# Optimization experiments

Measured on AMD Instinct MI355X. Metric: run time of the kernel, lower is better.

## Reference

```python
import jax, jax.numpy as jnp
import numpy as np

B, S, M, E, H = 2, 2048, 2048, 1024, 16
D = E // H
LN_EPS = 1e-5


def setup_inputs() -> dict:
    key = jax.random.key(0)
    ks = jax.random.split(key, 14)
    w = lambda k: jax.random.normal(k, (E, E), dtype=jnp.float32) * 0.02
    return {
        "query": jax.random.normal(ks[0], (B, S, E), dtype=jnp.float32),
        "keys": jax.random.normal(ks[1], (B, M, E), dtype=jnp.float32),
        "values": jax.random.normal(ks[2], (B, M, E), dtype=jnp.float32),
        "Wq": w(ks[3]), "bq": jnp.zeros((E,), jnp.float32),
        "Wk": w(ks[4]), "bk": jnp.zeros((E,), jnp.float32),
        "Wv": w(ks[5]), "bv": jnp.zeros((E,), jnp.float32),
        "Wo": w(ks[6]), "bo": jnp.zeros((E,), jnp.float32),
        "gamma": jnp.ones((E,), jnp.float32),
        "beta": jnp.zeros((E,), jnp.float32),
    }


def reference(query, keys, values, Wq, bq, Wk, bk, Wv, bv, Wo, bo, gamma, beta):
    b, s, e = query.shape
    m = keys.shape[1]
    # projections (torch Linear: x @ W.T + b), split heads -> [b, H, len, D]
    Q = (jnp.einsum('bse,fe->bsf', query, Wq) + bq).reshape(b, s, H, D).transpose(0, 2, 1, 3)
    K = (jnp.einsum('bme,fe->bmf', keys, Wk) + bk).reshape(b, m, H, D).transpose(0, 2, 1, 3)
    V = (jnp.einsum('bme,fe->bmf', values, Wv) + bv).reshape(b, m, H, D).transpose(0, 2, 1, 3)
    scores = jnp.einsum('bhsd,bhmd->bhsm', Q, K) / np.sqrt(D).astype(np.float32)
    attn = jax.nn.softmax(scores, axis=-1)  # [b,H,s,m]; dropout is eval no-op
    attended = jnp.einsum('bhsm,bhmd->bhsd', attn, V)
    attended = attended.transpose(0, 2, 1, 3).reshape(b, s, e)
    y = jnp.einsum('bse,fe->bsf', attended, Wo) + bo + query
    mu = jnp.mean(y, axis=-1, keepdims=True)
    var = jnp.mean(jnp.square(y - mu), axis=-1, keepdims=True)
    out = (y - mu) * jax.lax.rsqrt(var + LN_EPS) * gamma + beta
    avg_attention = attn.mean(axis=1)  # [b,s,m]
    return out, avg_attention
```

## Files before the change

kernel.cpp:

```cpp
#include <hip/hip_runtime.h>
#include <hip/hip_bf16.h>

typedef unsigned short u16;
typedef unsigned int   u32;
typedef __attribute__((ext_vector_type(2)))  float fx2;
typedef __attribute__((ext_vector_type(4)))  float fx4;
typedef __attribute__((ext_vector_type(16))) float f32x16;
typedef __attribute__((ext_vector_type(4)))  u16   usx4;
typedef __attribute__((ext_vector_type(8)))  u16   usx8;
typedef __attribute__((ext_vector_type(8)))  __bf16 bf16x8;
typedef __attribute__((ext_vector_type(2)))  int   i32x2;
typedef __attribute__((ext_vector_type(2)))  u32   u32x2;

#define DEVI static __device__ __forceinline__

constexpr int Bb = 2, Ss = 2048, Mm = 2048, Ee = 1024, Hh = 16, Dd = 64;
#define QSCALE 0.18033688011112042f

DEVI u16 f2bf(float f) {
  u32 u = __builtin_bit_cast(u32, f);
  u32 r = (u + 0x7fffu + ((u >> 16) & 1u)) >> 16;
  return (u16)r;
}
DEVI bf16x8 as_bf(usx8 v) { return __builtin_bit_cast(bf16x8, v); }

DEVI void gld16(const u16* g, u16* l) {
  __builtin_amdgcn_global_load_lds((const __attribute__((address_space(1))) void*)g,
                                   (__attribute__((address_space(3))) void*)l, 16, 0, 0);
}

#if __has_builtin(__builtin_amdgcn_exp2f)
DEVI float xexp2(float x) { return __builtin_amdgcn_exp2f(x); }
#else
DEVI float xexp2(float x) { return exp2f(x); }
#endif

DEVI u32 cvtpk(float lo, float hi) {
  u32 r;
  asm("v_cvt_pk_bf16_f32 %0, %1, %2" : "=v"(r) : "v"(lo), "v"(hi));
  return r;
}
DEVI bf16x8 pa_from(u32 w0, u32 w1, u32 w2, u32 w3) {
  union { u32 u[4]; usx8 v; } t;
  t.u[0] = w0; t.u[1] = w1; t.u[2] = w2; t.u[3] = w3;
  return as_bf(t.v);
}

__global__ __launch_bounds__(256)
void gemm_qkv(const float* __restrict__ query, const float* __restrict__ keys,
              const float* __restrict__ values,
              const float* __restrict__ Wq, const float* __restrict__ bq,
              const float* __restrict__ Wk, const float* __restrict__ bk,
              const float* __restrict__ Wv, const float* __restrict__ bv,
              u16* __restrict__ Qbf, u16* __restrict__ Kbf, u16* __restrict__ Vt)
{
  __shared__ u16 As[2][128][40];
  __shared__ u16 Bs[2][64][40];
  const int tid = threadIdx.x;
  const int w = tid >> 6, l = tid & 63, g = l >> 4, ln = l & 15;
  const int wr = w >> 1, wc = w & 1;
  const int row0 = blockIdx.y * 128, col0 = blockIdx.x * 64;
  const int z = blockIdx.z;

  const float* A = (z == 0) ? query : (z == 1) ? keys : values;
  const float* W = (z == 0) ? Wq : (z == 1) ? Wk : Wv;
  const float* bias = (z == 0) ? bq : (z == 1) ? bk : bv;

  fx4 ra[4]; fx4 rb[2];
  auto g2r = [&](int kt) {
#pragma unroll
    for (int i = 0; i < 4; i++) {
      int f = tid + i * 256;
      int rr = f >> 3, c4 = f & 7;
      ra[i] = *(const fx4*)(A + (size_t)(row0 + rr) * 1024 + kt * 32 + c4 * 4);
    }
#pragma unroll
    for (int i = 0; i < 2; i++) {
      int f = tid + i * 256;
      int rr = f >> 3, c4 = f & 7;
      rb[i] = *(const fx4*)(W + (size_t)(col0 + rr) * 1024 + kt * 32 + c4 * 4);
    }
  };
  auto r2l = [&](int buf) {
#pragma unroll
    for (int i = 0; i < 4; i++) {
      int f = tid + i * 256;
      int rr = f >> 3, c4 = f & 7;
      u32x2 ua;
      ua[0] = cvtpk(ra[i][0], ra[i][1]); ua[1] = cvtpk(ra[i][2], ra[i][3]);
      *(u32x2*)&As[buf][rr][c4 * 4] = ua;
    }
#pragma unroll
    for (int i = 0; i < 2; i++) {
      int f = tid + i * 256;
      int rr = f >> 3, c4 = f & 7;
      u32x2 ub;
      ub[0] = cvtpk(rb[i][0], rb[i][1]); ub[1] = cvtpk(rb[i][2], rb[i][3]);
      *(u32x2*)&Bs[buf][rr][c4 * 4] = ub;
    }
  };

  fx4 acc[4][2];
#pragma unroll
  for (int i = 0; i < 4; i++)
#pragma unroll
    for (int j = 0; j < 2; j++) acc[i][j] = fx4{0.f, 0.f, 0.f, 0.f};

  g2r(0); r2l(0);
  const int NK = 1024 / 32;
  for (int kt = 0; kt < NK; kt++) {
    __syncthreads();
    if (kt + 1 < NK) g2r(kt + 1);
    const int buf = kt & 1;
    bf16x8 af[4], bfr[2];
#pragma unroll
    for (int mi = 0; mi < 4; mi++)
      af[mi] = as_bf(*(const usx8*)&As[buf][wr * 64 + mi * 16 + ln][g * 8]);
#pragma unroll
    for (int nj = 0; nj < 2; nj++)
      bfr[nj] = as_bf(*(const usx8*)&Bs[buf][wc * 32 + nj * 16 + ln][g * 8]);
    __builtin_amdgcn_s_setprio(1);
#pragma unroll
    for (int mi = 0; mi < 4; mi++)
#pragma unroll
      for (int nj = 0; nj < 2; nj++)
        acc[mi][nj] = __builtin_amdgcn_mfma_f32_16x16x32_bf16(af[mi], bfr[nj], acc[mi][nj], 0, 0, 0);
    __builtin_amdgcn_s_setprio(0);
    if (kt + 1 < NK) r2l((kt + 1) & 1);
  }

#pragma unroll
  for (int mi = 0; mi < 4; mi++) {
#pragma unroll
    for (int nj = 0; nj < 2; nj++) {
      const int j = col0 + wc * 32 + nj * 16 + ln;
      const float bj = bias[j];
      if (z == 2) {
        const int i0 = row0 + wr * 64 + mi * 16 + g * 4;
        const int b2 = i0 >> 11, m2 = i0 & 2047;
        const int h2 = j >> 6,  d2 = j & 63;
        u32x2 pk;
        pk[0] = cvtpk(acc[mi][nj][0] + bj, acc[mi][nj][1] + bj);
        pk[1] = cvtpk(acc[mi][nj][2] + bj, acc[mi][nj][3] + bj);
        *(u32x2*)&Vt[(((size_t)b2 * Hh + h2) * 64 + d2) * (size_t)Mm + m2] = pk;
      } else {
        u16* outp = (z == 0) ? Qbf : Kbf;
        const float sc = (z == 0) ? QSCALE : 1.0f;
#pragma unroll
        for (int r = 0; r < 4; r++) {
          const int i = row0 + wr * 64 + mi * 16 + g * 4 + r;
          outp[(size_t)i * 1024 + j] = f2bf((acc[mi][nj][r] + bj) * sc);
        }
      }
    }
  }
}

__global__ __launch_bounds__(256)
void gemm_out(const u16* __restrict__ Ab, const float* __restrict__ W,
              const float* __restrict__ bias, const float* __restrict__ resid,
              float* __restrict__ outf)
{
  __shared__ u16 As[2][128][40];
  __shared__ u16 Bs[2][64][40];
  const int tid = threadIdx.x;
  const int w = tid >> 6, l = tid & 63, g = l >> 4, ln = l & 15;
  const int wr = w >> 1, wc = w & 1;
  const int row0 = blockIdx.y * 128, col0 = blockIdx.x * 64;

  usx4 rau[4]; fx4 rb[2];
  auto g2r = [&](int kt) {
#pragma unroll
    for (int i = 0; i < 4; i++) {
      int f = tid + i * 256;
      int rr = f >> 3, c4 = f & 7;
      rau[i] = *(const usx4*)(Ab + (size_t)(row0 + rr) * 1024 + kt * 32 + c4 * 4);
    }
#pragma unroll
    for (int i = 0; i < 2; i++) {
      int f = tid + i * 256;
      int rr = f >> 3, c4 = f & 7;
      rb[i] = *(const fx4*)(W + (size_t)(col0 + rr) * 1024 + kt * 32 + c4 * 4);
    }
  };
  auto r2l = [&](int buf) {
#pragma unroll
    for (int i = 0; i < 4; i++) {
      int f = tid + i * 256;
      int rr = f >> 3, c4 = f & 7;
      *(usx4*)&As[buf][rr][c4 * 4] = rau[i];
    }
#pragma unroll
    for (int i = 0; i < 2; i++) {
      int f = tid + i * 256;
      int rr = f >> 3, c4 = f & 7;
      u32x2 ub;
      ub[0] = cvtpk(rb[i][0], rb[i][1]); ub[1] = cvtpk(rb[i][2], rb[i][3]);
      *(u32x2*)&Bs[buf][rr][c4 * 4] = ub;
    }
  };

  fx4 acc[4][2];
#pragma unroll
  for (int i = 0; i < 4; i++)
#pragma unroll
    for (int j = 0; j < 2; j++) acc[i][j] = fx4{0.f, 0.f, 0.f, 0.f};

  g2r(0); r2l(0);
  const int NK = 1024 / 32;
  for (int kt = 0; kt < NK; kt++) {
    __syncthreads();
    if (kt + 1 < NK) g2r(kt + 1);
    const int buf = kt & 1;
    bf16x8 af[4], bfr[2];
#pragma unroll
    for (int mi = 0; mi < 4; mi++)
      af[mi] = as_bf(*(const usx8*)&As[buf][wr * 64 + mi * 16 + ln][g * 8]);
#pragma unroll
    for (int nj = 0; nj < 2; nj++)
      bfr[nj] = as_bf(*(const usx8*)&Bs[buf][wc * 32 + nj * 16 + ln][g * 8]);
    __builtin_amdgcn_s_setprio(1);
#pragma unroll
    for (int mi = 0; mi < 4; mi++)
#pragma unroll
      for (int nj = 0; nj < 2; nj++)
        acc[mi][nj] = __builtin_amdgcn_mfma_f32_16x16x32_bf16(af[mi], bfr[nj], acc[mi][nj], 0, 0, 0);
    __builtin_amdgcn_s_setprio(0);
    if (kt + 1 < NK) r2l((kt + 1) & 1);
  }

#pragma unroll
  for (int mi = 0; mi < 4; mi++) {
#pragma unroll
    for (int nj = 0; nj < 2; nj++) {
      const int j = col0 + wc * 32 + nj * 16 + ln;
      const float bj = bias[j];
#pragma unroll
      for (int r = 0; r < 4; r++) {
        const int i = row0 + wr * 64 + mi * 16 + g * 4 + r;
        float v = acc[mi][nj][r] + bj + resid[(size_t)i * 1024 + j];
        outf[(size_t)i * 1024 + j] = v;
      }
    }
  }
}

__global__ __launch_bounds__(256, 2)
void flash_fwd(const u16* __restrict__ Qb, const u16* __restrict__ Kb,
               const u16* __restrict__ Vt, u16* __restrict__ attended,
               float* __restrict__ stats)
{
  __shared__ u16 Ks[2][128][64];
  __shared__ u16 Vs[2][64][128];
  const int tid = threadIdx.x;
  const int w = tid >> 6, l = tid & 63;
  const int ln32 = l & 31, hi = l >> 5;
  const int st = blockIdx.x, h = blockIdx.y, b = blockIdx.z;
  const int s0 = st * 128 + w * 32;

  const u16* Kbase = Kb + (size_t)b * Mm * 1024 + h * 64;
  const u16* Vbase = Vt + ((size_t)(b * Hh + h) * 64) * (size_t)Mm;

  const int colu_k = (((l & 7) ^ (l >> 3)) << 3);
  auto stage = [&](int buf, int mt) {
    const int mb = mt * 128;
#pragma unroll
    for (int j = 0; j < 4; j++) {
      const int c = j * 4 + w;
      const int krow = c * 8 + (l >> 3);
      gld16(Kbase + (size_t)(mb + krow) * 1024 + colu_k,
            &Ks[buf][0][0] + c * 512 + l * 8);
      const int vrow = c * 4 + (l >> 4);
      const int colv = (((l & 15) ^ (vrow & 15)) << 3);
      gld16(Vbase + (size_t)vrow * (size_t)Mm + mb + colv,
            &Vs[buf][0][0] + c * 512 + l * 8);
    }
  };

  bf16x8 qa[4];
#pragma unroll
  for (int dstep = 0; dstep < 4; dstep++)
    qa[dstep] = as_bf(*(const usx8*)(Qb + (size_t)(b * Ss + s0 + ln32) * Ee
                                     + h * 64 + dstep * 16 + hi * 8));

  f32x16 acc[2];
#pragma unroll
  for (int i = 0; i < 16; i++) { acc[0][i] = 0.f; acc[1][i] = 0.f; }
  float lsum = 0.f;

  stage(0, 0);
  __syncthreads();

  const int NT = Mm / 128;
  for (int mt = 0; mt < NT; mt++) {
    const int buf = mt & 1;
    if (mt + 1 < NT) stage(buf ^ 1, mt + 1);

    f32x16 sc[4];
#pragma unroll
    for (int mtile = 0; mtile < 4; mtile++) {
      const int row = mtile * 32 + ln32;
      const int sw = (row & 7) << 3;
      f32x16 c;
#pragma unroll
      for (int i = 0; i < 16; i++) c[i] = 0.f;
#pragma unroll
      for (int dstep = 0; dstep < 4; dstep++) {
        bf16x8 kf = as_bf(*(const usx8*)&Ks[buf][row][(dstep * 16 + hi * 8) ^ sw]);
        c = __builtin_amdgcn_mfma_f32_32x32x16_bf16(kf, qa[dstep], c, 0, 0, 0);
      }
      sc[mtile] = c;
    }

#pragma unroll
    for (int mtile = 0; mtile < 4; mtile++) {
      float p[16];
#pragma unroll
      for (int r = 0; r < 16; r++) p[r] = xexp2(sc[mtile][r]);
      float t0 = (p[0] + p[1]) + (p[2] + p[3]);
      float t1 = (p[4] + p[5]) + (p[6] + p[7]);
      float t2 = (p[8] + p[9]) + (p[10] + p[11]);
      float t3 = (p[12] + p[13]) + (p[14] + p[15]);
      lsum += (t0 + t1) + (t2 + t3);

      u32 cp[8];
#pragma unroll
      for (int i = 0; i < 8; i++) cp[i] = cvtpk(p[2 * i], p[2 * i + 1]);
      i32x2 sA = __builtin_amdgcn_permlane32_swap((int)cp[0], (int)cp[2], false, false);
      i32x2 sB = __builtin_amdgcn_permlane32_swap((int)cp[1], (int)cp[3], false, false);
      bf16x8 pa0 = pa_from((u32)sA.x, (u32)sB.x, (u32)sA.y, (u32)sB.y);
      i32x2 sC = __builtin_amdgcn_permlane32_swap((int)cp[4], (int)cp[6], false, false);
      i32x2 sD = __builtin_amdgcn_permlane32_swap((int)cp[5], (int)cp[7], false, false);
      bf16x8 pa1 = pa_from((u32)sC.x, (u32)sD.x, (u32)sC.y, (u32)sD.y);

#pragma unroll
      for (int dtile = 0; dtile < 2; dtile++) {
        const int vrow = dtile * 32 + ln32;
        const int vsw = (vrow & 15) << 3;
        bf16x8 vb0 = as_bf(*(const usx8*)&Vs[buf][vrow][(mtile * 32 + hi * 8) ^ vsw]);
        bf16x8 vb1 = as_bf(*(const usx8*)&Vs[buf][vrow][(mtile * 32 + 16 + hi * 8) ^ vsw]);
        acc[dtile] = __builtin_amdgcn_mfma_f32_32x32x16_bf16(pa0, vb0, acc[dtile], 0, 0, 0);
        acc[dtile] = __builtin_amdgcn_mfma_f32_32x32x16_bf16(pa1, vb1, acc[dtile], 0, 0, 0);
      }
    }
    __syncthreads();
  }

  lsum += __shfl_xor(lsum, 32);
  const float inv = 1.0f / lsum;
  if (l < 32)
    stats[(size_t)(b * Hh + h) * Ss + s0 + l] = inv;
#pragma unroll
  for (int r = 0; r < 16; r++) {
    const int srow = (r & 3) + 8 * (r >> 2) + 4 * hi;
    const float invr = __shfl(inv, srow);
    const int s_abs = s0 + srow;
#pragma unroll
    for (int dtile = 0; dtile < 2; dtile++)
      attended[(size_t)(b * Ss + s_abs) * Ee + h * 64 + dtile * 32 + ln32] =
          f2bf(acc[dtile][r] * invr);
  }
}

__global__ __launch_bounds__(256)
void avg_attn(const u16* __restrict__ Qb, const u16* __restrict__ Kb,
              const float* __restrict__ stats, float* __restrict__ avg_out)
{
  __shared__ u16 Ks[2][64][64];
  const int tid = threadIdx.x;
  const int w = tid >> 6, l = tid & 63;
  const int ln32 = l & 31, hi = l >> 5;
  const int mtile0 = blockIdx.x, stile = blockIdx.y, b = blockIdx.z;
  const int m0 = mtile0 * 64;
  const int s0 = stile * 128 + w * 32;
  const int s_lane = s0 + ln32;

  const u16* Kbase = Kb + (size_t)(b * Mm + m0) * 1024;
  const u16* Qrow  = Qb + (size_t)(b * Ss + s_lane) * Ee;
  const float* strow = stats + (size_t)b * Hh * Ss + s_lane;

  const int colu = (((l & 7) ^ (l >> 3)) << 3);
  auto stage = [&](int buf, int h) {
#pragma unroll
    for (int j = 0; j < 2; j++) {
      const int c = j * 4 + w;
      const int row = c * 8 + (l >> 3);
      u16* kdst = &Ks[buf][0][0] + c * 512 + l * 8;
      gld16(Kbase + (size_t)row * 1024 + h * 64 + colu, kdst);
    }
  };

  f32x16 acc[2];
#pragma unroll
  for (int i = 0; i < 16; i++) { acc[0][i] = 0.f; acc[1][i] = 0.f; }

  stage(0, 0);
  __syncthreads();

  for (int h = 0; h < Hh; h++) {
    const int buf = h & 1;
    if (h + 1 < Hh) stage(buf ^ 1, h + 1);

    bf16x8 qa[4];
#pragma unroll
    for (int dstep = 0; dstep < 4; dstep++)
      qa[dstep] = as_bf(*(const usx8*)(Qrow + h * 64 + dstep * 16 + hi * 8));
    const float invh = strow[(size_t)h * Ss];

#pragma unroll
    for (int mtile = 0; mtile < 2; mtile++) {
      const int row = mtile * 32 + ln32;
      const int sw = (row & 7) << 3;
      f32x16 c;
#pragma unroll
      for (int i = 0; i < 16; i++) c[i] = 0.f;
      __builtin_amdgcn_s_setprio(1);
#pragma unroll
      for (int dstep = 0; dstep < 4; dstep++) {
        bf16x8 kf = as_bf(*(const usx8*)&Ks[buf][row][(dstep * 16 + hi * 8) ^ sw]);
        c = __builtin_amdgcn_mfma_f32_32x32x16_bf16(kf, qa[dstep], c, 0, 0, 0);
      }
      __builtin_amdgcn_s_setprio(0);
#pragma unroll
      for (int r = 0; r < 16; r++)
        acc[mtile][r] += xexp2(c[r]) * invh;
    }
    __syncthreads();
  }

  float* orow = avg_out + ((size_t)(b * Ss + s_lane)) * Mm + m0;
#pragma unroll
  for (int mtile = 0; mtile < 2; mtile++)
#pragma unroll
    for (int rq = 0; rq < 4; rq++) {
      fx4 o;
#pragma unroll
      for (int j = 0; j < 4; j++) o[j] = acc[mtile][rq * 4 + j] * (1.0f / 16.0f);
      *(fx4*)(orow + mtile * 32 + rq * 8 + 4 * hi) = o;
    }
}

__global__ __launch_bounds__(256)
void ln_kernel(const float* __restrict__ y, const float* __restrict__ gamma,
               const float* __restrict__ beta, float* __restrict__ out)
{
  const int row = blockIdx.x, tid = threadIdx.x;
  const int w = tid >> 6, l = tid & 63;
  fx4 v = *(const fx4*)(y + (size_t)row * 1024 + tid * 4);
  float s = v[0] + v[1] + v[2] + v[3];
  float s2 = v[0] * v[0] + v[1] * v[1] + v[2] * v[2] + v[3] * v[3];
#pragma unroll
  for (int off = 32; off >= 1; off >>= 1) {
    s += __shfl_xor(s, off);
    s2 += __shfl_xor(s2, off);
  }
  __shared__ float rs[4], rq[4];
  if (l == 0) { rs[w] = s; rq[w] = s2; }
  __syncthreads();
  s = (rs[0] + rs[1]) + (rs[2] + rs[3]);
  s2 = (rq[0] + rq[1]) + (rq[2] + rq[3]);
  const float mu = s * (1.0f / 1024.0f);
  const float var = s2 * (1.0f / 1024.0f) - mu * mu;
  const float rstd = rsqrtf(var + 1e-5f);
  fx4 gm = *(const fx4*)(gamma + tid * 4);
  fx4 bt = *(const fx4*)(beta + tid * 4);
  fx4 o;
#pragma unroll
  for (int j = 0; j < 4; j++) o[j] = (v[j] - mu) * rstd * gm[j] + bt[j];
  *(fx4*)(out + (size_t)row * 1024 + tid * 4) = o;
}

extern "C" void kernel_launch(void* const* d_in, const int* in_sizes, int n_in,
                              void* d_out, int out_size, void* d_ws, size_t ws_size,
                              hipStream_t stream)
{
  const float* query = (const float*)d_in[0];
  const float* keys  = (const float*)d_in[1];
  const float* values = (const float*)d_in[2];
  const float* Wq = (const float*)d_in[3];  const float* bq = (const float*)d_in[4];
  const float* Wk = (const float*)d_in[5];  const float* bk = (const float*)d_in[6];
  const float* Wv = (const float*)d_in[7];  const float* bv = (const float*)d_in[8];
  const float* Wo = (const float*)d_in[9];  const float* bo = (const float*)d_in[10];
  const float* gamma = (const float*)d_in[11];
  const float* beta  = (const float*)d_in[12];

  float* out = (float*)d_out;
  float* avg_out = out + (size_t)Bb * Ss * Ee;

  char* ws = (char*)d_ws;
  u16*   Qbf      = (u16*)(ws);
  u16*   Kbf      = (u16*)(ws + (size_t)8  * 1024 * 1024);
  u16*   Vt       = (u16*)(ws + (size_t)16 * 1024 * 1024);
  u16*   att_bf   = (u16*)(ws + (size_t)24 * 1024 * 1024);
  float* stats    = (float*)(ws + (size_t)40 * 1024 * 1024);
  float* ybuf     = (float*)(ws);

  gemm_qkv<<<dim3(16, 32, 3), 256, 0, stream>>>(query, keys, values,
                                                Wq, bq, Wk, bk, Wv, bv,
                                                Qbf, Kbf, Vt);

  flash_fwd<<<dim3(Ss / 128, Hh, Bb), 256, 0, stream>>>(Qbf, Kbf, Vt, att_bf, stats);
  avg_attn<<<dim3(Mm / 64, Ss / 128, Bb), 256, 0, stream>>>(Qbf, Kbf, stats, avg_out);

  gemm_out<<<dim3(16, 32, 1), 256, 0, stream>>>(att_bf, Wo, bo, query, ybuf);
  ln_kernel<<<dim3(Bb * Ss), 256, 0, stream>>>(ybuf, gamma, beta, out);
}
```

Measured before the change: 189.6 us.

## Pre-cast inputs and weights to bf16, use direct-to-LDS loads with larger GEMM tiles

Adds a cast kernel that converts the activations and all four weight matrices to bf16 before the projections. The QKV and output GEMMs then stage tiles with global_load_lds into XOR-swizzled shared memory, move from 128x64 to 128x128 tiles with a K-step of 64, and remap block IDs to group the work. This removes the register round-trip and the per-tile fp32-to-bf16 conversion in the GEMM inner loops. In exchange it adds a separate pass that reads the fp32 inputs and writes bf16 copies, plus more workspace memory. The weights are re-cast on every call.

```diff
diff --git a/kernel.cpp b/kernel.cpp
--- a/kernel.cpp
+++ b/kernel.cpp
@@ -11,6 +11,7 @@
 typedef __attribute__((ext_vector_type(8)))  __bf16 bf16x8;
 typedef __attribute__((ext_vector_type(2)))  int   i32x2;
 typedef __attribute__((ext_vector_type(2)))  u32   u32x2;
+typedef __attribute__((ext_vector_type(4)))  u32   u32x4;
 
 #define DEVI static __device__ __forceinline__
 
@@ -47,93 +48,117 @@
 }
 
 __global__ __launch_bounds__(256)
-void gemm_qkv(const float* __restrict__ query, const float* __restrict__ keys,
-              const float* __restrict__ values,
-              const float* __restrict__ Wq, const float* __restrict__ bq,
-              const float* __restrict__ Wk, const float* __restrict__ bk,
-              const float* __restrict__ Wv, const float* __restrict__ bv,
+void cast_all(const float* __restrict__ q, const float* __restrict__ k,
+              const float* __restrict__ v,
+              const float* __restrict__ wq, const float* __restrict__ wk,
+              const float* __restrict__ wv, const float* __restrict__ wo,
+              u16* __restrict__ qc, u16* __restrict__ kc, u16* __restrict__ vc,
+              u16* __restrict__ wqc, u16* __restrict__ wkc,
+              u16* __restrict__ wvc, u16* __restrict__ woc)
+{
+  const int y = blockIdx.y;
+  const float* s; u16* d; size_t n;
+  const size_t NI = (size_t)Bb * Ss * Ee;
+  const size_t NW = (size_t)Ee * Ee;
+  switch (y) {
+    case 0: s = q;  d = qc;  n = NI; break;
+    case 1: s = k;  d = kc;  n = NI; break;
+    case 2: s = v;  d = vc;  n = NI; break;
+    case 3: s = wq; d = wqc; n = NW; break;
+    case 4: s = wk; d = wkc; n = NW; break;
+    case 5: s = wv; d = wvc; n = NW; break;
+    default: s = wo; d = woc; n = NW; break;
+  }
+  const size_t stride = (size_t)gridDim.x * 256 * 8;
+  for (size_t i = ((size_t)blockIdx.x * 256 + threadIdx.x) * 8; i < n; i += stride) {
+    fx4 a = *(const fx4*)(s + i);
+    fx4 b = *(const fx4*)(s + i + 4);
+    u32x4 o;
+    o[0] = cvtpk(a[0], a[1]); o[1] = cvtpk(a[2], a[3]);
+    o[2] = cvtpk(b[0], b[1]); o[3] = cvtpk(b[2], b[3]);
+    *(u32x4*)(d + i) = o;
+  }
+}
+
+__global__ __launch_bounds__(256, 2)
+void gemm_qkv(const u16* __restrict__ qc, const u16* __restrict__ kc,
+              const u16* __restrict__ vc,
+              const u16* __restrict__ wqc, const u16* __restrict__ wkc,
+              const u16* __restrict__ wvc,
+              const float* __restrict__ bq, const float* __restrict__ bk,
+              const float* __restrict__ bv,
               u16* __restrict__ Qbf, u16* __restrict__ Kbf, u16* __restrict__ Vt)
 {
-  __shared__ u16 As[2][128][40];
-  __shared__ u16 Bs[2][64][40];
+  __shared__ u16 As[2][128][64];
+  __shared__ u16 Bs[2][128][64];
   const int tid = threadIdx.x;
   const int w = tid >> 6, l = tid & 63, g = l >> 4, ln = l & 15;
   const int wr = w >> 1, wc = w & 1;
-  const int row0 = blockIdx.y * 128, col0 = blockIdx.x * 64;
-  const int z = blockIdx.z;
-
-  const float* A = (z == 0) ? query : (z == 1) ? keys : values;
-  const float* W = (z == 0) ? Wq : (z == 1) ? Wk : Wv;
+
+  const int lid = blockIdx.x;
+  const int wg = (lid & 7) * 96 + (lid >> 3);
+  const int z = wg >> 8;
+  const int rem = wg & 255;
+  const int row0 = (rem >> 3) * 128;
+  const int col0 = (rem & 7) * 128;
+
+  const u16* A = (z == 0) ? qc : (z == 1) ? kc : vc;
+  const u16* W = (z == 0) ? wqc : (z == 1) ? wkc : wvc;
   const float* bias = (z == 0) ? bq : (z == 1) ? bk : bv;
 
-  fx4 ra[4]; fx4 rb[2];
-  auto g2r = [&](int kt) {
-#pragma unroll
-    for (int i = 0; i < 4; i++) {
-      int f = tid + i * 256;
-      int rr = f >> 3, c4 = f & 7;
-      ra[i] = *(const fx4*)(A + (size_t)(row0 + rr) * 1024 + kt * 32 + c4 * 4);
-    }
-#pragma unroll
-    for (int i = 0; i < 2; i++) {
-      int f = tid + i * 256;
-      int rr = f >> 3, c4 = f & 7;
-      rb[i] = *(const fx4*)(W + (size_t)(col0 + rr) * 1024 + kt * 32 + c4 * 4);
+  const int colu = (((l & 7) ^ (l >> 3)) << 3);
+  auto stage = [&](int buf, int kt) {
+#pragma unroll
+    for (int j = 0; j < 4; j++) {
+      const int c = j * 4 + w;
+      const int row = c * 8 + (l >> 3);
+      gld16(A + (size_t)(row0 + row) * 1024 + kt * 64 + colu,
+            &As[buf][0][0] + c * 512 + l * 8);
+      gld16(W + (size_t)(col0 + row) * 1024 + kt * 64 + colu,
+            &Bs[buf][0][0] + c * 512 + l * 8);
     }
   };
-  auto r2l = [&](int buf) {
-#pragma unroll
-    for (int i = 0; i < 4; i++) {
-      int f = tid + i * 256;
-      int rr = f >> 3, c4 = f & 7;
-      u32x2 ua;
-      ua[0] = cvtpk(ra[i][0], ra[i][1]); ua[1] = cvtpk(ra[i][2], ra[i][3]);
-      *(u32x2*)&As[buf][rr][c4 * 4] = ua;
-    }
-#pragma unroll
-    for (int i = 0; i < 2; i++) {
-      int f = tid + i * 256;
-      int rr = f >> 3, c4 = f & 7;
-      u32x2 ub;
-      ub[0] = cvtpk(rb[i][0], rb[i][1]); ub[1] = cvtpk(rb[i][2], rb[i][3]);
-      *(u32x2*)&Bs[buf][rr][c4 * 4] = ub;
-    }
-  };
-
-  fx4 acc[4][2];
+
+  fx4 acc[4][4];
 #pragma unroll
   for (int i = 0; i < 4; i++)
 #pragma unroll
-    for (int j = 0; j < 2; j++) acc[i][j] = fx4{0.f, 0.f, 0.f, 0.f};
-
-  g2r(0); r2l(0);
-  const int NK = 1024 / 32;
+    for (int j = 0; j < 4; j++) acc[i][j] = fx4{0.f, 0.f, 0.f, 0.f};
+
+  stage(0, 0);
+  __syncthreads();
+
+  const int swA = (ln & 7) << 3;
+  const int NK = 1024 / 64;
   for (int kt = 0; kt < NK; kt++) {
+    const int buf = kt & 1;
+    if (kt + 1 < NK) stage(buf ^ 1, kt + 1);
+#pragma unroll
+    for (int ks = 0; ks < 2; ks++) {
+      bf16x8 af[4], bfr[4];
+      const int cb = (ks * 32 + g * 8) ^ swA;
+#pragma unroll
+      for (int mi = 0; mi < 4; mi++)
+        af[mi] = as_bf(*(const usx8*)&As[buf][wr * 64 + mi * 16 + ln][cb]);
+#pragma unroll
+      for (int nj = 0; nj < 4; nj++)
+        bfr[nj] = as_bf(*(const usx8*)&Bs[buf][wc * 64 + nj * 16 + ln][cb]);
+      __builtin_amdgcn_s_setprio(1);
+#pragma unroll
+      for (int mi = 0; mi < 4; mi++)
+#pragma unroll
+        for (int nj = 0; nj < 4; nj++)
+          acc[mi][nj] = __builtin_amdgcn_mfma_f32_16x16x32_bf16(af[mi], bfr[nj], acc[mi][nj], 0, 0, 0);
+      __builtin_amdgcn_s_setprio(0);
+    }
     __syncthreads();
-    if (kt + 1 < NK) g2r(kt + 1);
-    const int buf = kt & 1;
-    bf16x8 af[4], bfr[2];
-#pragma unroll
-    for (int mi = 0; mi < 4; mi++)
-      af[mi] = as_bf(*(const usx8*)&As[buf][wr * 64 + mi * 16 + ln][g * 8]);
-#pragma unroll
-    for (int nj = 0; nj < 2; nj++)
-      bfr[nj] = as_bf(*(const usx8*)&Bs[buf][wc * 32 + nj * 16 + ln][g * 8]);
-    __builtin_amdgcn_s_setprio(1);
-#pragma unroll
-    for (int mi = 0; mi < 4; mi++)
-#pragma unroll
-      for (int nj = 0; nj < 2; nj++)
-        acc[mi][nj] = __builtin_amdgcn_mfma_f32_16x16x32_bf16(af[mi], bfr[nj], acc[mi][nj], 0, 0, 0);
-    __builtin_amdgcn_s_setprio(0);
-    if (kt + 1 < NK) r2l((kt + 1) & 1);
   }
 
 #pragma unroll
   for (int mi = 0; mi < 4; mi++) {
 #pragma unroll
-    for (int nj = 0; nj < 2; nj++) {
-      const int j = col0 + wc * 32 + nj * 16 + ln;
+    for (int nj = 0; nj < 4; nj++) {
+      const int j = col0 + wc * 64 + nj * 16 + ln;
       const float bj = bias[j];
       if (z == 2) {
         const int i0 = row0 + wr * 64 + mi * 16 + g * 4;
@@ -156,90 +181,80 @@
   }
 }
 
-__global__ __launch_bounds__(256)
-void gemm_out(const u16* __restrict__ Ab, const float* __restrict__ W,
+__global__ __launch_bounds__(256, 2)
+void gemm_out(const u16* __restrict__ Ab, const u16* __restrict__ W,
               const float* __restrict__ bias, const float* __restrict__ resid,
               float* __restrict__ outf)
 {
-  __shared__ u16 As[2][128][40];
-  __shared__ u16 Bs[2][64][40];
+  __shared__ u16 As[2][128][64];
+  __shared__ u16 Bs[2][128][64];
   const int tid = threadIdx.x;
   const int w = tid >> 6, l = tid & 63, g = l >> 4, ln = l & 15;
   const int wr = w >> 1, wc = w & 1;
-  const int row0 = blockIdx.y * 128, col0 = blockIdx.x * 64;
-
-  usx4 rau[4]; fx4 rb[2];
-  auto g2r = [&](int kt) {
-#pragma unroll
-    for (int i = 0; i < 4; i++) {
-      int f = tid + i * 256;
-      int rr = f >> 3, c4 = f & 7;
-      rau[i] = *(const usx4*)(Ab + (size_t)(row0 + rr) * 1024 + kt * 32 + c4 * 4);
-    }
-#pragma unroll
-    for (int i = 0; i < 2; i++) {
-      int f = tid + i * 256;
-      int rr = f >> 3, c4 = f & 7;
-      rb[i] = *(const fx4*)(W + (size_t)(col0 + rr) * 1024 + kt * 32 + c4 * 4);
+
+  const int lid = blockIdx.x;
+  const int wg = (lid & 7) * 32 + (lid >> 3);
+  const int row0 = (wg >> 3) * 128;
+  const int col0 = (wg & 7) * 128;
+
+  const int colu = (((l & 7) ^ (l >> 3)) << 3);
+  auto stage = [&](int buf, int kt) {
+#pragma unroll
+    for (int j = 0; j < 4; j++) {
+      const int c = j * 4 + w;
+      const int row = c * 8 + (l >> 3);
+      gld16(Ab + (size_t)(row0 + row) * 1024 + kt * 64 + colu,
+            &As[buf][0][0] + c * 512 + l * 8);
+      gld16(W + (size_t)(col0 + row) * 1024 + kt * 64 + colu,
+            &Bs[buf][0][0] + c * 512 + l * 8);
     }
   };
-  auto r2l = [&](int buf) {
-#pragma unroll
-    for (int i = 0; i < 4; i++) {
-      int f = tid + i * 256;
-      int rr = f >> 3, c4 = f & 7;
-      *(usx4*)&As[buf][rr][c4 * 4] = rau[i];
-    }
-#pragma unroll
-    for (int i = 0; i < 2; i++) {
-      int f = tid + i * 256;
-      int rr = f >> 3, c4 = f & 7;
-      u32x2 ub;
-      ub[0] = cvtpk(rb[i][0], rb[i][1]); ub[1] = cvtpk(rb[i][2], rb[i][3]);
-      *(u32x2*)&Bs[buf][rr][c4 * 4] = ub;
-    }
-  };
-
-  fx4 acc[4][2];
+
+  fx4 acc[4][4];
 #pragma unroll
   for (int i = 0; i < 4; i++)
 #pragma unroll
-    for (int j = 0; j < 2; j++) acc[i][j] = fx4{0.f, 0.f, 0.f, 0.f};
-
-  g2r(0); r2l(0);
-  const int NK = 1024 / 32;
+    for (int j = 0; j < 4; j++) acc[i][j] = fx4{0.f, 0.f, 0.f, 0.f};
+
+  stage(0, 0);
+  __syncthreads();
+
+  const int swA = (ln & 7) << 3;
+  const int NK = 1024 / 64;
   for (int kt = 0; kt < NK; kt++) {
+    const int buf = kt & 1;
+    if (kt + 1 < NK) stage(buf ^ 1, kt + 1);
+#pragma unroll
+    for (int ks = 0; ks < 2; ks++) {
+      bf16x8 af[4], bfr[4];
+      const int cb = (ks * 32 + g * 8) ^ swA;
+#pragma unroll
+      for (int mi = 0; mi < 4; mi++)
+        af[mi] = as_bf(*(const usx8*)&As[buf][wr * 64 + mi * 16 + ln][cb]);
+#pragma unroll
+      for (int nj = 0; nj < 4; nj++)
+        bfr[nj] = as_bf(*(const usx8*)&Bs[buf][wc * 64 + nj * 16 + ln][cb]);
+      __builtin_amdgcn_s_setprio(1);
+#pragma unroll
+      for (int mi = 0; mi < 4; mi++)
+#pragma unroll
+        for (int nj = 0; nj < 4; nj++)
+          acc[mi][nj] = __builtin_amdgcn_mfma_f32_16x16x32_bf16(af[mi], bfr[nj], acc[mi][nj], 0, 0, 0);
+      __builtin_amdgcn_s_setprio(0);
+    }
     __syncthreads();
-    if (kt + 1 < NK) g2r(kt + 1);
-    const int buf = kt & 1;
-    bf16x8 af[4], bfr[2];
-#pragma unroll
-    for (int mi = 0; mi < 4; mi++)
-      af[mi] = as_bf(*(const usx8*)&As[buf][wr * 64 + mi * 16 + ln][g * 8]);
-#pragma unroll
-    for (int nj = 0; nj < 2; nj++)
-      bfr[nj] = as_bf(*(const usx8*)&Bs[buf][wc * 32 + nj * 16 + ln][g * 8]);
-    __builtin_amdgcn_s_setprio(1);
-#pragma unroll
-    for (int mi = 0; mi < 4; mi++)
-#pragma unroll
-      for (int nj = 0; nj < 2; nj++)
-        acc[mi][nj] = __builtin_amdgcn_mfma_f32_16x16x32_bf16(af[mi], bfr[nj], acc[mi][nj], 0, 0, 0);
-    __builtin_amdgcn_s_setprio(0);
-    if (kt + 1 < NK) r2l((kt + 1) & 1);
   }
 
 #pragma unroll
   for (int mi = 0; mi < 4; mi++) {
 #pragma unroll
-    for (int nj = 0; nj < 2; nj++) {
-      const int j = col0 + wc * 32 + nj * 16 + ln;
+    for (int nj = 0; nj < 4; nj++) {
+      const int j = col0 + wc * 64 + nj * 16 + ln;
       const float bj = bias[j];
 #pragma unroll
       for (int r = 0; r < 4; r++) {
         const int i = row0 + wr * 64 + mi * 16 + g * 4 + r;
-        float v = acc[mi][nj][r] + bj + resid[(size_t)i * 1024 + j];
-        outf[(size_t)i * 1024 + j] = v;
+        outf[(size_t)i * 1024 + j] = acc[mi][nj][r] + bj + resid[(size_t)i * 1024 + j];
       }
     }
   }
@@ -487,21 +502,31 @@
   float* out = (float*)d_out;
   float* avg_out = out + (size_t)Bb * Ss * Ee;
 
+  const size_t MB = 1024 * 1024;
   char* ws = (char*)d_ws;
-  u16*   Qbf      = (u16*)(ws);
-  u16*   Kbf      = (u16*)(ws + (size_t)8  * 1024 * 1024);
-  u16*   Vt       = (u16*)(ws + (size_t)16 * 1024 * 1024);
-  u16*   att_bf   = (u16*)(ws + (size_t)24 * 1024 * 1024);
-  float* stats    = (float*)(ws + (size_t)40 * 1024 * 1024);
-  float* ybuf     = (float*)(ws);
-
-  gemm_qkv<<<dim3(16, 32, 3), 256, 0, stream>>>(query, keys, values,
-                                                Wq, bq, Wk, bk, Wv, bv,
-                                                Qbf, Kbf, Vt);
+  u16*   Qbf    = (u16*)(ws);
+  u16*   Kbf    = (u16*)(ws + 8  * MB);
+  u16*   Vt     = (u16*)(ws + 16 * MB);
+  u16*   qc     = (u16*)(ws + 24 * MB);
+  u16*   kc     = (u16*)(ws + 32 * MB);
+  u16*   vc     = (u16*)(ws + 40 * MB);
+  u16*   wqc    = (u16*)(ws + 48 * MB);
+  u16*   wkc    = (u16*)(ws + 50 * MB);
+  u16*   wvc    = (u16*)(ws + 52 * MB);
+  u16*   woc    = (u16*)(ws + 54 * MB);
+  float* stats  = (float*)(ws + 56 * MB);
+  u16*   att_bf = (u16*)(ws + 24 * MB);
+  float* ybuf   = (float*)(ws);
+
+  cast_all<<<dim3(512, 7), 256, 0, stream>>>(query, keys, values, Wq, Wk, Wv, Wo,
+                                             qc, kc, vc, wqc, wkc, wvc, woc);
+
+  gemm_qkv<<<dim3(768), 256, 0, stream>>>(qc, kc, vc, wqc, wkc, wvc,
+                                          bq, bk, bv, Qbf, Kbf, Vt);
 
   flash_fwd<<<dim3(Ss / 128, Hh, Bb), 256, 0, stream>>>(Qbf, Kbf, Vt, att_bf, stats);
   avg_attn<<<dim3(Mm / 64, Ss / 128, Bb), 256, 0, stream>>>(Qbf, Kbf, stats, avg_out);
 
-  gemm_out<<<dim3(16, 32, 1), 256, 0, stream>>>(att_bf, Wo, bo, query, ybuf);
+  gemm_out<<<dim3(256), 256, 0, stream>>>(att_bf, woc, bo, query, ybuf);
   ln_kernel<<<dim3(Bb * Ss), 256, 0, stream>>>(ybuf, gamma, beta, out);
 }
```

Measured after the change: 173.5 us. 8.5% less time.
